# Performance work log

Hardware: AMD Instinct MI355X
Metric: run time of the kernel (lower is better)

The kernel has to match this reference:

```python
import jax, jax.numpy as jnp
import numpy as np
from jax import lax

T, B, INPUT, HID, OUT, FUT = 128, 1024, 4, 512, 4, 32


def setup_inputs() -> dict:
    key = jax.random.key(0)
    ks = jax.random.split(key, 12)
    s = 0.05  # small init like uniform(-1/sqrt(H), 1/sqrt(H))
    inp = {
        "x": jax.random.normal(ks[0], (T, B, INPUT), jnp.float32),
        "Wih1": jax.random.normal(ks[1], (4 * HID, INPUT), jnp.float32) * s,
        "Whh1": jax.random.normal(ks[2], (4 * HID, HID), jnp.float32) * s,
        "bih1": jax.random.normal(ks[3], (4 * HID,), jnp.float32) * s,
        "bhh1": jax.random.normal(ks[4], (4 * HID,), jnp.float32) * s,
        "Wih2": jax.random.normal(ks[5], (4 * HID, HID), jnp.float32) * s,
        "Whh2": jax.random.normal(ks[6], (4 * HID, HID), jnp.float32) * s,
        "bih2": jax.random.normal(ks[7], (4 * HID,), jnp.float32) * s,
        "bhh2": jax.random.normal(ks[8], (4 * HID,), jnp.float32) * s,
        "Wl": jax.random.normal(ks[9], (OUT, HID), jnp.float32) * s,
        "bl": jax.random.normal(ks[10], (OUT,), jnp.float32) * s,
        "future": FUT,
    }
    return inp


def _cell(xt, h, c, Wih, Whh, bih, bhh):
    # PyTorch LSTMCell gate order: i, f, g, o
    g = xt @ Wih.T + bih + h @ Whh.T + bhh  # [B, 4H]
    i, f, gg, o = jnp.split(g, 4, axis=-1)
    c = jax.nn.sigmoid(f) * c + jax.nn.sigmoid(i) * jnp.tanh(gg)
    h = jax.nn.sigmoid(o) * jnp.tanh(c)
    return h, c


def reference(x, Wih1, Whh1, bih1, bhh1, Wih2, Whh2, bih2, bhh2, Wl, bl, future):
    nb = x.shape[1]
    H = Whh1.shape[1]
    z = jnp.zeros((nb, H), x.dtype)

    def step1(carry, xt):
        h1, c1, h2, c2 = carry
        h1, c1 = _cell(xt, h1, c1, Wih1, Whh1, bih1, bhh1)
        h2, c2 = _cell(h1, h2, c2, Wih2, Whh2, bih2, bhh2)
        return (h1, c1, h2, c2), None

    (h1, c1, h2, c2), _ = lax.scan(step1, (z, z, z, z), x)
    tmp_out = h2  # frozen last hidden of cell 2 (faithful to original bug)

    def step2(carry, _):
        h1, c1, h2, c2 = carry
        # original future loop reuses lstm2 weights for both updates
        h1, c1 = _cell(tmp_out, h1, c1, Wih2, Whh2, bih2, bhh2)
        h2, c2 = _cell(h1, h2, c2, Wih2, Whh2, bih2, bhh2)
        out = h2 @ Wl.T + bl  # [B, OUT]
        return (h1, c1, h2, c2), out

    _, outs = lax.scan(step2, (h1, c1, h2, c2), None, length=future)
    return outs  # [future, B, OUT]
```

## Files before the change

### kernel.cpp

```cpp
#include <hip/hip_runtime.h>

typedef _Float16 v8h __attribute__((ext_vector_type(8)));
typedef float v4f __attribute__((ext_vector_type(4)));
typedef unsigned int uint;

#define OFF_BAR   0
#define OFF_AO0   4096
#define OFF_AO1   (OFF_AO0 + (1<<21))
#define OFF_AF0   (OFF_AO1 + (1<<21))
#define OFF_AF1   (OFF_AF0 + (1<<21))
#define OFF_W1    (OFF_AF1 + (1<<21))
#define OFF_W2    (OFF_W1 + (1<<21))
#define OFF_B1    (OFF_W2 + (1<<22))
#define OFF_B2    (OFF_B1 + 8192)

__global__ __launch_bounds__(256, 1)
void lstm_prep(const float* __restrict__ Whh1, const float* __restrict__ Wih2,
               const float* __restrict__ Whh2, const float* __restrict__ bih1,
               const float* __restrict__ bhh1, const float* __restrict__ bih2,
               const float* __restrict__ bhh2,
               _Float16* __restrict__ W1p, _Float16* __restrict__ W2p,
               float* __restrict__ bs1, float* __restrict__ bs2)
{
  const int total = 1048576 + 2097152 + 4096;
  for (int i = blockIdx.x*blockDim.x + threadIdx.x; i < total; i += gridDim.x*blockDim.x) {
    if (i < 1048576) {
      int nt = i >> 13, rem = i & 8191;
      int k32 = rem >> 9, c = rem & 511;
      int lane = c >> 3, el = c & 7;
      int n = nt*16 + (lane & 15);
      int k = k32*32 + (lane >> 4)*8 + el;
      W1p[i] = (_Float16)Whh1[n*512 + k];
    } else if (i < 3145728) {
      int j = i - 1048576;
      int nt = j >> 14, rem = j & 16383;
      int k32 = rem >> 9, c = rem & 511;
      int lane = c >> 3, el = c & 7;
      int n = nt*16 + (lane & 15);
      int k = k32*32 + (lane >> 4)*8 + el;
      float v = (k < 512) ? Wih2[n*512 + k] : Whh2[n*512 + (k - 512)];
      W2p[j] = (_Float16)v;
    } else {
      int n = i - 3145728;
      if (n < 2048) bs1[n] = bih1[n] + bhh1[n];
      else          bs2[n-2048] = bih2[n-2048] + bhh2[n-2048];
    }
  }
}

__device__ __forceinline__ float sigmoidf_(float z) { return 1.f / (1.f + __expf(-z)); }
__device__ __forceinline__ float tanhf_(float z)    { return 1.f - 2.f/(1.f + __expf(2.f*z)); }

__device__ __forceinline__ v8h ld_frag_dev(const _Float16* base, uint off) {
  union { unsigned long long u[2]; v8h h; } cv;
  const unsigned long long* q = (const unsigned long long*)(base + off);
  cv.u[0] = __hip_atomic_load(q,     __ATOMIC_RELAXED, __HIP_MEMORY_SCOPE_AGENT);
  cv.u[1] = __hip_atomic_load(q + 1, __ATOMIC_RELAXED, __HIP_MEMORY_SCOPE_AGENT);
  return cv.h;
}

__global__ __launch_bounds__(256, 2)
void lstm_main(const float* __restrict__ x, const float* __restrict__ Wih1,
               const float* __restrict__ Wl, const float* __restrict__ blv,
               _Float16* __restrict__ AO0, _Float16* __restrict__ AO1,
               _Float16* __restrict__ AF0, _Float16* __restrict__ AF1,
               const _Float16* __restrict__ W1, const _Float16* __restrict__ W2,
               const float* __restrict__ bs1, const float* __restrict__ bs2,
               int* __restrict__ bar, float* __restrict__ out)
{
  __shared__ float lred[14336];
  const int tid  = threadIdx.x;
  const int wv   = tid >> 6, lane = tid & 63;
  const int quad = lane >> 4, lc = lane & 15;
  const int kh   = wv >> 1;
  const int cw   = (wv & 1) ^ kh;
  const int bid  = blockIdx.x;
  const int jg   = bid >> 3;
  const int ht   = (bid & 7)*2 + (jg & 1);
  const int bt   = jg >> 1;

  _Float16* const AOv[2] = {AO0, AO1};
  _Float16* const AFv[2] = {AF0, AF1};

  const int erow = tid >> 3, enib = tid & 7;
  const int tid2  = tid - 128;
  const int b_loc = (tid2 >= 0) ? (tid2 >> 2) : 0, oct = tid2 & 3;
  const int m     = b_loc & 15, mtile_e = bt*2 + (b_loc >> 4);
  const int STASH = 8448;

  int ntg_[8];
  #pragma unroll
  for (int tt = 0; tt < 8; tt++) ntg_[tt] = (tt>>1)*32 + ht*2 + (tt&1);

  float c1s[4], c2s[4];
  #pragma unroll
  for (int i = 0; i < 4; i++) { c1s[i] = 0.f; c2s[i] = 0.f; }

  for (int r = 0; r < 162; r++) {
    const bool p1 = r < 129;
    const int  f  = r - 129;
    const int  wp = p1 ? (r & 1) : (f & 1);
    const int  rp = wp ^ 1;
    const _Float16* A1 = p1 ? AOv[rp] : AFv[rp];
    const _Float16* A2 = AOv[rp];
    const bool skip1 = (r == 128 || r == 161);
    const bool skip2 = (r == 0   || r == 129);

    const _Float16* Ac = cw ? A2 : A1;
    const _Float16* Bc = cw ? W2 : (p1 ? W1 : W2);
    const int wk   = cw ? 32 : (p1 ? 16 : 32);
    const int half = cw ? 16 : (p1 ? 8 : 16);
    const int ch0  = kh * half;

    v4f acc[2][8];
    #pragma unroll
    for (int i2 = 0; i2 < 2; i2++)
      #pragma unroll
      for (int tt = 0; tt < 8; tt++) acc[i2][tt] = (v4f){0,0,0,0};

    uint aoff[2];
    #pragma unroll
    for (int i2 = 0; i2 < 2; i2++)
      aoff[i2] = (uint)(((bt*2 + i2)*32 + ch0)*512 + lane*8);
    uint boff[8];
    #pragma unroll
    for (int tt = 0; tt < 8; tt++)
      boff[tt] = (uint)((ntg_[tt]*wk + ch0)*512 + lane*8);

    #pragma unroll 4
    for (int cc = 0; cc < half; cc++) {
      v8h av[2];
      #pragma unroll
      for (int i2 = 0; i2 < 2; i2++)
        av[i2] = ld_frag_dev(Ac, aoff[i2] + cc*512);
      #pragma unroll
      for (int tt = 0; tt < 8; tt++) {
        v8h bv = *(const v8h*)(Bc + boff[tt] + cc*512);
        #pragma unroll
        for (int i2 = 0; i2 < 2; i2++)
          acc[i2][tt] = __builtin_amdgcn_mfma_f32_16x16x32_f16(av[i2], bv, acc[i2][tt], 0, 0, 0);
      }
    }

    const int rbase = cw * 4096;
    if (kh) {
      #pragma unroll
      for (int i2 = 0; i2 < 2; i2++)
        #pragma unroll
        for (int tt = 0; tt < 8; tt++)
          *(v4f*)&lred[rbase + ((i2*8 + tt)*64 + lane)*4] = acc[i2][tt];
    }
    __syncthreads();
    if (!kh) {
      #pragma unroll
      for (int i2 = 0; i2 < 2; i2++)
        #pragma unroll
        for (int tt = 0; tt < 8; tt++)
          acc[i2][tt] += *(const v4f*)&lred[rbase + ((i2*8 + tt)*64 + lane)*4];
    }
    __syncthreads();

    if (!kh && cw == 0) {
      #pragma unroll
      for (int i2 = 0; i2 < 2; i2++)
        #pragma unroll
        for (int tt = 0; tt < 8; tt++) {
          int row = i2*16 + quad*4;
          int col = tt*16 + lc;
          #pragma unroll
          for (int rr = 0; rr < 4; rr++) lred[(row + rr)*132 + col] = acc[i2][tt][rr];
        }
    }
    __syncthreads();

    {
      const float* bsx = p1 ? bs1 : bs2;
      float g[4][4];
      #pragma unroll
      for (int g4 = 0; g4 < 4; g4++) {
        v4f gv = *(const v4f*)&lred[erow*132 + g4*32 + enib*4];
        v4f bv = *(const v4f*)&bsx[g4*512 + ht*32 + enib*4];
        #pragma unroll
        for (int j = 0; j < 4; j++) g[g4][j] = gv[j] + bv[j];
      }
      if (p1 && r < 128) {
        const v4f xv = *(const v4f*)(x + ((size_t)r*1024 + bt*32 + erow)*4);
        #pragma unroll
        for (int g4 = 0; g4 < 4; g4++)
          #pragma unroll
          for (int j = 0; j < 4; j++) {
            int hh = ht*32 + enib*4 + j;
            const v4f w = *(const v4f*)(Wih1 + (size_t)(g4*512 + hh)*4);
            g[g4][j] += xv[0]*w[0] + xv[1]*w[1] + xv[2]*w[2] + xv[3]*w[3];
          }
      }
      if (!skip1) {
        v4f hf;
        #pragma unroll
        for (int j = 0; j < 4; j++) {
          float ig = sigmoidf_(g[0][j]), fg = sigmoidf_(g[1][j]);
          float gg = tanhf_(g[2][j]),    og = sigmoidf_(g[3][j]);
          float c = fg*c1s[j] + ig*gg;
          c1s[j] = c;
          hf[j] = og * tanhf_(c);
        }
        *(v4f*)&lred[STASH + erow*36 + enib*4] = hf;
      }
    }
    __syncthreads();

    if (tid >= 128 && !skip1) {
      v4f h0 = *(const v4f*)&lred[STASH + b_loc*36 + oct*8];
      v4f h1 = *(const v4f*)&lred[STASH + b_loc*36 + oct*8 + 4];
      union { _Float16 h8[8]; unsigned long long u[2]; } hu;
      #pragma unroll
      for (int j = 0; j < 4; j++) { hu.h8[j] = (_Float16)h0[j]; hu.h8[4+j] = (_Float16)h1[j]; }
      auto st16 = [&](_Float16* bp, int chunk) {
        unsigned long long* p = (unsigned long long*)
          (bp + (((size_t)(mtile_e*32 + chunk)) << 9) + (oct*16 + m)*8);
        __hip_atomic_store(p,     hu.u[0], __ATOMIC_RELAXED, __HIP_MEMORY_SCOPE_AGENT);
        __hip_atomic_store(p + 1, hu.u[1], __ATOMIC_RELAXED, __HIP_MEMORY_SCOPE_AGENT);
      };
      if (p1) {
        st16(AOv[wp], ht);
        if (r == 127) st16(AFv[1], 16 + ht);
      } else {
        st16(AFv[wp], 16 + ht);
        st16(AOv[wp], ht);
      }
    }
    if (!kh && cw == 1) {
      #pragma unroll
      for (int i2 = 0; i2 < 2; i2++)
        #pragma unroll
        for (int tt = 0; tt < 8; tt++) {
          int row = i2*16 + quad*4;
          int col = tt*16 + lc;
          #pragma unroll
          for (int rr = 0; rr < 4; rr++) lred[(row + rr)*132 + col] = acc[i2][tt][rr];
        }
    }
    __syncthreads();

    {
      float g[4][4];
      #pragma unroll
      for (int g4 = 0; g4 < 4; g4++) {
        v4f gv = *(const v4f*)&lred[erow*132 + g4*32 + enib*4];
        v4f bv = *(const v4f*)&bs2[g4*512 + ht*32 + enib*4];
        #pragma unroll
        for (int j = 0; j < 4; j++) g[g4][j] = gv[j] + bv[j];
      }
      if (!skip2) {
        v4f hf;
        #pragma unroll
        for (int j = 0; j < 4; j++) {
          float ig = sigmoidf_(g[0][j]), fg = sigmoidf_(g[1][j]);
          float gg = tanhf_(g[2][j]),    og = sigmoidf_(g[3][j]);
          float c = fg*c2s[j] + ig*gg;
          c2s[j] = c;
          hf[j] = og * tanhf_(c);
        }
        *(v4f*)&lred[STASH + erow*36 + enib*4] = hf;
      }
    }
    __syncthreads();

    if (tid >= 128 && !skip2) {
      v4f h0 = *(const v4f*)&lred[STASH + b_loc*36 + oct*8];
      v4f h1 = *(const v4f*)&lred[STASH + b_loc*36 + oct*8 + 4];
      union { _Float16 h8[8]; unsigned long long u[2]; } hu;
      #pragma unroll
      for (int j = 0; j < 4; j++) { hu.h8[j] = (_Float16)h0[j]; hu.h8[4+j] = (_Float16)h1[j]; }
      auto st16 = [&](_Float16* bp, int chunk) {
        unsigned long long* p = (unsigned long long*)
          (bp + (((size_t)(mtile_e*32 + chunk)) << 9) + (oct*16 + m)*8);
        __hip_atomic_store(p,     hu.u[0], __ATOMIC_RELAXED, __HIP_MEMORY_SCOPE_AGENT);
        __hip_atomic_store(p + 1, hu.u[1], __ATOMIC_RELAXED, __HIP_MEMORY_SCOPE_AGENT);
      };
      st16(AOv[wp], 16 + ht);
      if (r == 128) { st16(AFv[0], ht); st16(AFv[1], ht); }
    }
    if (tid < 128 && !p1 && r >= 130) {
      const int s = r - 130;
      int bb = tid >> 2, o = tid & 3;
      float sa = (ht == 0) ? blv[o] : 0.f;
      const float* wl = Wl + (size_t)o*512 + ht*32;
      #pragma unroll
      for (int jj = 0; jj < 32; jj++) sa += lred[STASH + bb*36 + jj] * wl[jj];
      atomicAdd(&out[(((size_t)s*1024) + bt*32 + bb)*4 + o], sa);
    }
    __syncthreads();

    if (tid == 0) {
      int* ctr = bar + bt*32;
      __hip_atomic_fetch_add(ctr, 1, __ATOMIC_RELAXED, __HIP_MEMORY_SCOPE_AGENT);
      const int target = 16*(r+1);
      while (__hip_atomic_load(ctr, __ATOMIC_RELAXED, __HIP_MEMORY_SCOPE_AGENT) < target)
        __builtin_amdgcn_s_sleep(1);
    }
    __syncthreads();
  }
}

extern "C" void kernel_launch(void* const* d_in, const int* in_sizes, int n_in,
                              void* d_out, int out_size, void* d_ws, size_t ws_size,
                              hipStream_t stream) {
  const float* x    = (const float*)d_in[0];
  const float* Wih1 = (const float*)d_in[1];
  const float* Whh1 = (const float*)d_in[2];
  const float* bih1 = (const float*)d_in[3];
  const float* bhh1 = (const float*)d_in[4];
  const float* Wih2 = (const float*)d_in[5];
  const float* Whh2 = (const float*)d_in[6];
  const float* bih2 = (const float*)d_in[7];
  const float* bhh2 = (const float*)d_in[8];
  const float* Wl   = (const float*)d_in[9];
  const float* bl   = (const float*)d_in[10];

  char* ws = (char*)d_ws;
  int*      bar = (int*)(ws + OFF_BAR);
  _Float16* AO0 = (_Float16*)(ws + OFF_AO0);
  _Float16* AO1 = (_Float16*)(ws + OFF_AO1);
  _Float16* AF0 = (_Float16*)(ws + OFF_AF0);
  _Float16* AF1 = (_Float16*)(ws + OFF_AF1);
  _Float16* W1p = (_Float16*)(ws + OFF_W1);
  _Float16* W2p = (_Float16*)(ws + OFF_W2);
  float*    bs1 = (float*)(ws + OFF_B1);
  float*    bs2 = (float*)(ws + OFF_B2);

  hipMemsetAsync(ws, 0, (size_t)OFF_W1, stream);
  hipMemsetAsync(d_out, 0, (size_t)out_size * sizeof(float), stream);

  lstm_prep<<<2048, 256, 0, stream>>>(Whh1, Wih2, Whh2, bih1, bhh1, bih2, bhh2,
                                      W1p, W2p, bs1, bs2);
  lstm_main<<<512, 256, 0, stream>>>(x, Wih1, Wl, bl, AO0, AO1, AF0, AF1,
                                     W1p, W2p, bs1, bs2, bar, (float*)d_out);
}
```

Measured before the change: 2.916 ms.

## Split waves by M-tile instead of K-half to drop LDS reduction

Each wave now owns one 16-row batch tile and walks the full K range, instead of splitting K across wave pairs and reducing partial sums through shared memory. This removes the LDS store/load reduction and two block barriers per step. In exchange each wave does twice as many B-fragment loads per MFMA, since B is no longer reused across two M tiles, and the K loop is twice as long per wave.

```diff
diff --git a/kernel.cpp b/kernel.cpp
--- a/kernel.cpp
+++ b/kernel.cpp
@@ -72,8 +72,8 @@
   const int tid  = threadIdx.x;
   const int wv   = tid >> 6, lane = tid & 63;
   const int quad = lane >> 4, lc = lane & 15;
-  const int kh   = wv >> 1;
-  const int cw   = (wv & 1) ^ kh;
+  const int cw   = wv & 1;
+  const int mtb  = wv >> 1;
   const int bid  = blockIdx.x;
   const int jg   = bid >> 3;
   const int ht   = (bid & 7)*2 + (jg & 1);
@@ -108,68 +108,48 @@
 
     const _Float16* Ac = cw ? A2 : A1;
     const _Float16* Bc = cw ? W2 : (p1 ? W1 : W2);
-    const int wk   = cw ? 32 : (p1 ? 16 : 32);
-    const int half = cw ? 16 : (p1 ? 8 : 16);
-    const int ch0  = kh * half;
-
-    v4f acc[2][8];
+    const int HF = cw ? 32 : (p1 ? 16 : 32);
+    const int HH = HF >> 1;
+
+    v4f acc0[8], acc1[8];
     #pragma unroll
-    for (int i2 = 0; i2 < 2; i2++)
-      #pragma unroll
-      for (int tt = 0; tt < 8; tt++) acc[i2][tt] = (v4f){0,0,0,0};
-
-    uint aoff[2];
-    #pragma unroll
-    for (int i2 = 0; i2 < 2; i2++)
-      aoff[i2] = (uint)(((bt*2 + i2)*32 + ch0)*512 + lane*8);
+    for (int tt = 0; tt < 8; tt++) { acc0[tt] = (v4f){0,0,0,0}; acc1[tt] = (v4f){0,0,0,0}; }
+
+    const uint aoff = (uint)(((bt*2 + mtb)*32)*512 + lane*8);
     uint boff[8];
     #pragma unroll
     for (int tt = 0; tt < 8; tt++)
-      boff[tt] = (uint)((ntg_[tt]*wk + ch0)*512 + lane*8);
+      boff[tt] = (uint)((ntg_[tt]*HF)*512 + lane*8);
 
     #pragma unroll 4
-    for (int cc = 0; cc < half; cc++) {
-      v8h av[2];
-      #pragma unroll
-      for (int i2 = 0; i2 < 2; i2++)
-        av[i2] = ld_frag_dev(Ac, aoff[i2] + cc*512);
+    for (int cc = 0; cc < HH; cc++) {
+      v8h av = ld_frag_dev(Ac, aoff + cc*512);
       #pragma unroll
       for (int tt = 0; tt < 8; tt++) {
         v8h bv = *(const v8h*)(Bc + boff[tt] + cc*512);
-        #pragma unroll
-        for (int i2 = 0; i2 < 2; i2++)
-          acc[i2][tt] = __builtin_amdgcn_mfma_f32_16x16x32_f16(av[i2], bv, acc[i2][tt], 0, 0, 0);
-      }
-    }
-
-    const int rbase = cw * 4096;
-    if (kh) {
-      #pragma unroll
-      for (int i2 = 0; i2 < 2; i2++)
-        #pragma unroll
-        for (int tt = 0; tt < 8; tt++)
-          *(v4f*)&lred[rbase + ((i2*8 + tt)*64 + lane)*4] = acc[i2][tt];
-    }
-    __syncthreads();
-    if (!kh) {
-      #pragma unroll
-      for (int i2 = 0; i2 < 2; i2++)
-        #pragma unroll
-        for (int tt = 0; tt < 8; tt++)
-          acc[i2][tt] += *(const v4f*)&lred[rbase + ((i2*8 + tt)*64 + lane)*4];
-    }
-    __syncthreads();
-
-    if (!kh && cw == 0) {
-      #pragma unroll
-      for (int i2 = 0; i2 < 2; i2++)
-        #pragma unroll
-        for (int tt = 0; tt < 8; tt++) {
-          int row = i2*16 + quad*4;
-          int col = tt*16 + lc;
-          #pragma unroll
-          for (int rr = 0; rr < 4; rr++) lred[(row + rr)*132 + col] = acc[i2][tt][rr];
-        }
+        acc0[tt] = __builtin_amdgcn_mfma_f32_16x16x32_f16(av, bv, acc0[tt], 0, 0, 0);
+      }
+    }
+    #pragma unroll 4
+    for (int cc = HH; cc < 2*HH; cc++) {
+      v8h av = ld_frag_dev(Ac, aoff + cc*512);
+      #pragma unroll
+      for (int tt = 0; tt < 8; tt++) {
+        v8h bv = *(const v8h*)(Bc + boff[tt] + cc*512);
+        acc1[tt] = __builtin_amdgcn_mfma_f32_16x16x32_f16(av, bv, acc1[tt], 0, 0, 0);
+      }
+    }
+    #pragma unroll
+    for (int tt = 0; tt < 8; tt++) acc0[tt] += acc1[tt];
+
+    if (cw == 0) {
+      #pragma unroll
+      for (int tt = 0; tt < 8; tt++) {
+        int row = mtb*16 + quad*4;
+        int col = tt*16 + lc;
+        #pragma unroll
+        for (int rr = 0; rr < 4; rr++) lred[(row + rr)*132 + col] = acc0[tt][rr];
+      }
     }
     __syncthreads();
 
@@ -229,16 +209,14 @@
         st16(AOv[wp], ht);
       }
     }
-    if (!kh && cw == 1) {
-      #pragma unroll
-      for (int i2 = 0; i2 < 2; i2++)
-        #pragma unroll
-        for (int tt = 0; tt < 8; tt++) {
-          int row = i2*16 + quad*4;
-          int col = tt*16 + lc;
-          #pragma unroll
-          for (int rr = 0; rr < 4; rr++) lred[(row + rr)*132 + col] = acc[i2][tt][rr];
-        }
+    if (cw == 1) {
+      #pragma unroll
+      for (int tt = 0; tt < 8; tt++) {
+        int row = mtb*16 + quad*4;
+        int col = tt*16 + lc;
+        #pragma unroll
+        for (int rr = 0; rr < 4; rr++) lred[(row + rr)*132 + col] = acc0[tt][rr];
+      }
     }
     __syncthreads();
 
```

Measured after the change: 4.890 ms. 1.68x slower.
